# Kernel optimization log

Hardware: AMD Instinct MI355X
Metric: run time of the kernel (lower is better)

## Reference

```python
import jax, jax.numpy as jnp
import numpy as np

N = 1_048_576   # nodes
E = 8_388_608   # edges
G = 32_768      # graphs
D = 9           # node embedding dim (hardcoded emb_dim=9 in source)
H = 2 * D       # GIN MLP hidden
L = 3           # num_layers
ATOM_V, BOND_V = 119, 6
BN_EPS = 1e-5


def setup_inputs() -> dict:
    key = jax.random.key(0)
    ks = jax.random.split(key, 12)
    f = lambda i, shape: jax.random.normal(ks[i], shape, jnp.float32) * 0.1
    return {
        'atom_emb': f(0, (9, ATOM_V, D)),
        'bond_emb': f(1, (L, 3, BOND_V, D)),
        'eps_gin': jnp.zeros((L,), jnp.float32),
        'W1': f(2, (L, D, H)), 'b1': jnp.zeros((L, H)),
        'bn1_g': jnp.ones((L, H)), 'bn1_b': jnp.zeros((L, H)),
        'W2': f(3, (L, H, D)), 'b2': jnp.zeros((L, D)),
        'bno_g': jnp.ones((L, D)), 'bno_b': jnp.zeros((L, D)),
        'vnW1': f(4, (L - 1, D, H)), 'vnb1': jnp.zeros((L - 1, H)),
        'vnbn1_g': jnp.ones((L - 1, H)), 'vnbn1_b': jnp.zeros((L - 1, H)),
        'vnW2': f(5, (L - 1, H, D)), 'vnb2': jnp.zeros((L - 1, D)),
        'vnbn2_g': jnp.ones((L - 1, D)), 'vnbn2_b': jnp.zeros((L - 1, D)),
        'x': jax.random.randint(ks[6], (N, 9), 0, 2),
        'edge_index': jax.random.randint(ks[7], (2, E), 0, N),
        'edge_attr': jax.random.randint(ks[8], (E, 3), 0, 2),
        'batch': jnp.sort(jax.random.randint(ks[9], (N,), 0, G)),
        'num_graphs': G,
    }


def _bn(h, g, b):
    # BatchNorm1d in training mode: batch mean / biased variance
    m = h.mean(axis=0)
    v = h.var(axis=0)
    return (h - m) * jax.lax.rsqrt(v + BN_EPS) * g + b


def reference(atom_emb, bond_emb, eps_gin, W1, b1, bn1_g, bn1_b, W2, b2,
              bno_g, bno_b, vnW1, vnb1, vnbn1_g, vnbn1_b, vnW2, vnb2,
              vnbn2_g, vnbn2_b, x, edge_index, edge_attr, batch, num_graphs):
    n_nodes = x.shape[0]
    src, dst = edge_index[0], edge_index[1]
    # AtomEncoder: sum of per-field embeddings -> [N, D]
    h = atom_emb[jnp.arange(atom_emb.shape[0])[None, :], x].sum(axis=1)
    vn = jnp.zeros((num_graphs, h.shape[1]), h.dtype)  # virtualnode emb init 0
    num_layers = W1.shape[0]
    for l in range(num_layers):
        h_in = h + vn[batch]                              # broadcast VN to nodes
        # BondEncoder for this layer -> [E, D]
        e = bond_emb[l][jnp.arange(3)[None, :], edge_attr].sum(axis=1)
        # GIN message: relu(x_j + e), sum-aggregate at target
        msg = jax.nn.relu(h_in[src] + e)
        aggr = jax.ops.segment_sum(msg, dst, num_segments=n_nodes)
        z = (1.0 + eps_gin[l]) * h_in + aggr
        z = jax.nn.relu(_bn(z @ W1[l] + b1[l], bn1_g[l], bn1_b[l])) @ W2[l] + b2[l]
        z = _bn(z, bno_g[l], bno_b[l])
        if l < num_layers - 1:
            z = jax.nn.relu(z)
        h_new = z + h_in                                   # residual=True
        if l < num_layers - 1:
            vn_tmp = jax.ops.segment_sum(h_in, batch, num_segments=num_graphs) + vn
            t = jax.nn.relu(_bn(vn_tmp @ vnW1[l] + vnb1[l], vnbn1_g[l], vnbn1_b[l]))
            t = jax.nn.relu(_bn(t @ vnW2[l] + vnb2[l], vnbn2_g[l], vnbn2_b[l]))
            vn = vn + t                                    # VN residual
        h = h_new
    pooled = jax.ops.segment_sum(h, batch, num_segments=num_graphs)  # global_add_pool
    return jnp.sum(pooled, axis=0, keepdims=True)          # [1, D]
```

## Files before the change

### kernel.cpp

```cpp
#include <hip/hip_runtime.h>
#include <hip/hip_fp8.h>

#define NN 1048576
#define NE 8388608
#define NG 32768
#define DD 9
#define SB 12
#define HH 18
#define BN_EPS 1e-5f

#define NPB 512
#define NB  2048
#define NGRP 64
#define P3MAX 5120

#define NSUM1 0
#define NSQ1  18
#define NSUM2 36
#define NSQ2  45
#define OUTS  54
#define VBASE 4096
#define VSUM1 (VBASE+0)
#define VSQ1  (VBASE+18)
#define VSUM2 (VBASE+36)
#define VSQ2  (VBASE+45)
#define STATS_FLOATS 4224

typedef float fv4 __attribute__((ext_vector_type(4)));

__device__ __forceinline__ float waveReduce(float v) {
#pragma unroll
  for (int off = 32; off > 0; off >>= 1) v += __shfl_down(v, off, 64);
  return v;
}
__device__ __forceinline__ unsigned f8enc(float f) {
  __hip_fp8_e4m3 v(f);
  return (unsigned)v.__x;
}
__device__ __forceinline__ float f8dec(unsigned b) {
  __hip_fp8_e4m3 v;
  v.__x = (__hip_fp8_storage_t)b;
  return (float)v;
}


__global__ void k_count(const int* __restrict__ ei, int* __restrict__ bucket_count) {
  __shared__ int hist[NB];
  for (int i = threadIdx.x; i < NB; i += 256) hist[i] = 0;
  __syncthreads();
  const int CH = NE / 2048;
  int base = blockIdx.x * CH;
  for (int i = threadIdx.x; i < CH; i += 256)
    atomicAdd(&hist[ei[NE + base + i] >> 9], 1);
  __syncthreads();
  for (int i = threadIdx.x; i < NB; i += 256)
    if (hist[i]) atomicAdd(&bucket_count[i], hist[i]);
}

__global__ void k_scan(const int* __restrict__ bucket_count, int* __restrict__ bucket_base,
                       int* __restrict__ bucket_cursor, int* __restrict__ group_cursor) {
  __shared__ int tsum[256];
  int tid = threadIdx.x;
  int c[8];
  int run = 0;
#pragma unroll
  for (int k = 0; k < 8; ++k) { c[k] = bucket_count[tid * 8 + k]; run += c[k]; }
  tsum[tid] = run;
  __syncthreads();
  for (int off = 1; off < 256; off <<= 1) {
    int v = (tid >= off) ? tsum[tid - off] : 0;
    __syncthreads();
    tsum[tid] += v;
    __syncthreads();
  }
  int excl = tsum[tid] - run;
  if ((tid & 3) == 0) group_cursor[(tid >> 2) * 16] = excl;
#pragma unroll
  for (int k = 0; k < 8; ++k) {
    bucket_base[tid * 8 + k] = excl;
    bucket_cursor[tid * 8 + k] = excl;
    excl += c[k];
  }
  if (tid == 255) bucket_base[NB] = tsum[255];
}

#define P1K 32
__global__ void __launch_bounds__(256)
k_p1(const int* __restrict__ ei, const int* __restrict__ ea,
     int* __restrict__ group_cursor, uint2* __restrict__ coarse) {
  __shared__ uint2 stage[NGRP * P1K];
  __shared__ int scnt[NGRP], gbase[NGRP];
  int tid = threadIdx.x;
  for (int i = tid; i < NGRP; i += 256) scnt[i] = 0;
  __syncthreads();
  const int CH = NE / 2048;
  int base = blockIdx.x * CH;
  for (int batch = 0; batch < CH / 1024; ++batch) {
#pragma unroll
    for (int k = 0; k < 4; ++k) {
      int e = base + batch * 1024 + k * 256 + tid;
      int s = ei[e];
      int d = ei[NE + e];
      unsigned at = (unsigned)((ea[(size_t)e * 3 + 0] & 1) |
                               ((ea[(size_t)e * 3 + 1] & 1) << 1) |
                               ((ea[(size_t)e * 3 + 2] & 1) << 2));
      int g = d >> 14;
      uint2 rec = make_uint2((unsigned)s | (at << 20), (unsigned)d);
      int pos = atomicAdd(&scnt[g], 1);
      if (pos < P1K) stage[g * P1K + pos] = rec;
      else coarse[atomicAdd(&group_cursor[g * 16], 1)] = rec;
    }
    __syncthreads();
    {
      int g = tid >> 2, j = tid & 3;
      int cnt = min(scnt[g], P1K);
      if (j == 0) gbase[g] = cnt ? atomicAdd(&group_cursor[g * 16], cnt) : 0;
      __syncthreads();
      for (int i = j; i < cnt; i += 4) coarse[gbase[g] + i] = stage[g * P1K + i];
    }
    __syncthreads();
    if (tid < NGRP) scnt[tid] = 0;
    __syncthreads();
  }
}

#define P2K 48
#define P2SUB 32
__global__ void __launch_bounds__(256)
k_p2(const uint2* __restrict__ coarse, const int* __restrict__ bucket_base,
     int* __restrict__ bucket_cursor, unsigned* __restrict__ binned) {
  __shared__ unsigned stage[32 * P2K];
  __shared__ int scnt[32], gbase[32];
  int tid = threadIdx.x;
  int g = blockIdx.x >> 5;
  int sub = blockIdx.x & 31;
  int s0 = bucket_base[g << 5];
  int s1 = bucket_base[(g + 1) << 5];
  int len = s1 - s0;
  int chunk = (len + P2SUB - 1) >> 5;
  int my0 = s0 + sub * chunk;
  int my1 = min(my0 + chunk, s1);
  if (tid < 32) scnt[tid] = 0;
  __syncthreads();
  for (int b0 = my0; b0 < my1; b0 += 1024) {
#pragma unroll
    for (int k = 0; k < 4; ++k) {
      int i = b0 + k * 256 + tid;
      if (i < my1) {
        uint2 rec = coarse[i];
        unsigned s = rec.x & 0xFFFFFu;
        unsigned at = rec.x >> 20;
        unsigned d = rec.y;
        int bt = (int)((d >> 9) & 31u);
        unsigned o = s | ((d & 511u) << 20) | (at << 29);
        int pos = atomicAdd(&scnt[bt], 1);
        if (pos < P2K) stage[bt * P2K + pos] = o;
        else binned[atomicAdd(&bucket_cursor[(g << 5) | bt], 1)] = o;
      }
    }
    __syncthreads();
    {
      int bt = tid >> 3, j = tid & 7;
      int cnt = min(scnt[bt], P2K);
      if (j == 0) gbase[bt] = cnt ? atomicAdd(&bucket_cursor[(g << 5) | bt], cnt) : 0;
      __syncthreads();
      for (int i = j; i < cnt; i += 8) binned[gbase[bt] + i] = stage[bt * P2K + i];
    }
    __syncthreads();
    if (tid < 32) scnt[tid] = 0;
    __syncthreads();
  }
}

__global__ void __launch_bounds__(256)
k_p3(unsigned* __restrict__ binned, const int* __restrict__ bucket_base,
     int* __restrict__ row_ptr) {
  __shared__ int cnt[512];
  __shared__ int tsum[256];
  __shared__ unsigned stage[P3MAX];
  int tid = threadIdx.x;
  int b = blockIdx.x;
  int s0 = bucket_base[b], s1 = bucket_base[b + 1];
  int len = s1 - s0;
  for (int i = tid; i < 512; i += 256) cnt[i] = 0;
  __syncthreads();
  for (int i = tid; i < len; i += 256) {
    unsigned rec = binned[s0 + i];
    atomicAdd(&cnt[(rec >> 20) & 511u], 1);
  }
  __syncthreads();
  int c0 = cnt[2 * tid], c1 = cnt[2 * tid + 1];
  int run = c0 + c1;
  tsum[tid] = run;
  __syncthreads();
  for (int off = 1; off < 256; off <<= 1) {
    int v = (tid >= off) ? tsum[tid - off] : 0;
    __syncthreads();
    tsum[tid] += v;
    __syncthreads();
  }
  int excl = tsum[tid] - run;
  row_ptr[b * NPB + 2 * tid] = s0 + excl;
  row_ptr[b * NPB + 2 * tid + 1] = s0 + excl + c0;
  if (b == NB - 1 && tid == 255) row_ptr[NN] = s0 + excl + c0 + c1;
  __syncthreads();
  cnt[2 * tid] = excl;
  cnt[2 * tid + 1] = excl + c0;
  __syncthreads();
  for (int i = tid; i < len; i += 256) {
    unsigned rec = binned[s0 + i];
    int pos = atomicAdd(&cnt[(rec >> 20) & 511u], 1);
    stage[pos] = (rec & 0xFFFFFu) | ((rec >> 29) << 20);
  }
  __syncthreads();
  for (int i = tid; i < len; i += 256) binned[s0 + i] = stage[i];
}


__device__ __forceinline__ void writeMirror(uint2* __restrict__ hmA,
                                            unsigned char* __restrict__ hmB,
                                            size_t n, const float* hv) {
  uint2 q;
  q.x = f8enc(hv[0]) | (f8enc(hv[1]) << 8) | (f8enc(hv[2]) << 16) | (f8enc(hv[3]) << 24);
  q.y = f8enc(hv[4]) | (f8enc(hv[5]) << 8) | (f8enc(hv[6]) << 16) | (f8enc(hv[7]) << 24);
  hmA[n] = q;
  hmB[n] = (unsigned char)f8enc(hv[8]);
}

__global__ void k_atom(const float* __restrict__ atom_emb, const int* __restrict__ x,
                       const int* __restrict__ batch, float* __restrict__ h,
                       uint2* __restrict__ hmA, unsigned char* __restrict__ hmB,
                       float* __restrict__ vnsum) {
  int n = blockIdx.x * 256 + threadIdx.x;
  int xi[9];
#pragma unroll
  for (int f = 0; f < 9; ++f) xi[f] = x[(size_t)n * 9 + f];
  float acc[DD] = {0.f,0.f,0.f,0.f,0.f,0.f,0.f,0.f,0.f};
#pragma unroll
  for (int f = 0; f < 9; ++f) {
    const float* row = atom_emb + ((size_t)f * 119 + xi[f]) * DD;
#pragma unroll
    for (int d = 0; d < DD; ++d) acc[d] += row[d];
  }
  float* o = h + (size_t)n * SB;
  ((float4*)o)[0] = make_float4(acc[0], acc[1], acc[2], acc[3]);
  ((float4*)o)[1] = make_float4(acc[4], acc[5], acc[6], acc[7]);
  o[8] = acc[8];
  writeMirror(hmA, hmB, (size_t)n, acc);
  int g = batch[n];
  int lane = threadIdx.x & 63;
  float s[DD];
#pragma unroll
  for (int d = 0; d < DD; ++d) s[d] = acc[d];
#pragma unroll
  for (int st = 1; st < 64; st <<= 1) {
    int gu = __shfl_up(g, st, 64);
    bool ok = (lane >= st) && (gu == g);
#pragma unroll
    for (int d = 0; d < DD; ++d) {
      float vu = __shfl_up(s[d], st, 64);
      if (ok) s[d] += vu;
    }
  }
  int gn = __shfl_down(g, 1, 64);
  if ((lane == 63) || (gn != g)) {
#pragma unroll
    for (int d = 0; d < DD; ++d) atomicAdd(&vnsum[(size_t)g * DD + d], s[d]);
  }
}

__device__ __forceinline__ void edgeDecodeAcc(unsigned r, uint2 q, unsigned db,
                                              const float* __restrict__ comb,
                                              float* __restrict__ acc) {
  const float* cb = comb + (r >> 20) * DD;
  float hv[DD] = {f8dec(q.x & 255u), f8dec((q.x >> 8) & 255u),
                  f8dec((q.x >> 16) & 255u), f8dec(q.x >> 24),
                  f8dec(q.y & 255u), f8dec((q.y >> 8) & 255u),
                  f8dec((q.y >> 16) & 255u), f8dec(q.y >> 24),
                  f8dec(db)};
#pragma unroll
  for (int d = 0; d < DD; ++d) {
    float m = hv[d] + cb[d];
    m = m > 0.f ? m : 0.f;
    acc[d] += m;
  }
}

__device__ __forceinline__ void accumNode(const unsigned* __restrict__ binned,
                                          int e0, int e1,
                                          const uint2* __restrict__ hmA,
                                          const unsigned char* __restrict__ hmB,
                                          const float* __restrict__ comb,
                                          float* __restrict__ acc) {
  int i = e0;
  for (; i + 4 <= e1; i += 4) {
    unsigned r0 = binned[i], r1 = binned[i + 1], r2 = binned[i + 2], r3 = binned[i + 3];
    uint2 q0 = hmA[r0 & 0xFFFFFu];
    uint2 q1 = hmA[r1 & 0xFFFFFu];
    uint2 q2 = hmA[r2 & 0xFFFFFu];
    uint2 q3 = hmA[r3 & 0xFFFFFu];
    unsigned char d0 = hmB[r0 & 0xFFFFFu];
    unsigned char d1 = hmB[r1 & 0xFFFFFu];
    unsigned char d2 = hmB[r2 & 0xFFFFFu];
    unsigned char d3 = hmB[r3 & 0xFFFFFu];
    edgeDecodeAcc(r0, q0, d0, comb, acc);
    edgeDecodeAcc(r1, q1, d1, comb, acc);
    edgeDecodeAcc(r2, q2, d2, comb, acc);
    edgeDecodeAcc(r3, q3, d3, comb, acc);
  }
  for (; i < e1; ++i) {
    unsigned r = binned[i];
    uint2 q = hmA[r & 0xFFFFFu];
    unsigned char db = hmB[r & 0xFFFFFu];
    edgeDecodeAcc(r, q, db, comb, acc);
  }
}

__global__ void __launch_bounds__(256, 8)
k_edgeA(const float* __restrict__ hbuf, const uint2* __restrict__ hmA,
        const unsigned char* __restrict__ hmB, const unsigned* __restrict__ binned,
        const int* __restrict__ row_ptr, const float* __restrict__ bond,
        const float* __restrict__ W1l, const float* __restrict__ b1l,
        const float* __restrict__ epsp, float* __restrict__ X,
        float* __restrict__ stats) {
  __shared__ float comb[8 * DD];
  __shared__ float sW1[DD * HH], sb1[HH], ssum[HH], ssq[HH];
  int tid = threadIdx.x;
  for (int i = tid; i < DD * HH; i += 256) sW1[i] = W1l[i];
  if (tid < 8 * DD) {
    int c = tid / DD, d = tid % DD;
    comb[tid] = bond[(0 * 6 + (c & 1)) * DD + d] +
                bond[(1 * 6 + ((c >> 1) & 1)) * DD + d] +
                bond[(2 * 6 + ((c >> 2) & 1)) * DD + d];
  }
  if (tid < HH) { sb1[tid] = b1l[tid]; ssum[tid] = 0.f; ssq[tid] = 0.f; }
  __syncthreads();

  int b = blockIdx.x;
  int nA = b * NPB + tid;
  int nB = nA + 256;
  int ea0 = row_ptr[nA], ea1 = row_ptr[nA + 1];
  int eb0 = row_ptr[nB], eb1 = row_ptr[nB + 1];
  float acc0[DD] = {0.f,0.f,0.f,0.f,0.f,0.f,0.f,0.f,0.f};
  float acc1[DD] = {0.f,0.f,0.f,0.f,0.f,0.f,0.f,0.f,0.f};
  accumNode(binned, ea0, ea1, hmA, hmB, comb, acc0);
  accumNode(binned, eb0, eb1, hmA, hmB, comb, acc1);

  float eps1 = 1.0f + epsp[0];
  float z0[DD], z1[DD];
  {
    const float* hr = hbuf + (size_t)nA * SB;
    float4 HA = ((const float4*)hr)[0], HB = ((const float4*)hr)[1];
    float h8 = hr[8];
    float hi[DD] = {HA.x, HA.y, HA.z, HA.w, HB.x, HB.y, HB.z, HB.w, h8};
#pragma unroll
    for (int d = 0; d < DD; ++d) z0[d] = eps1 * hi[d] + acc0[d];
    float* xo = X + (size_t)nA * SB;
    fv4 v0 = {z0[0], z0[1], z0[2], z0[3]};
    fv4 v1 = {z0[4], z0[5], z0[6], z0[7]};
    __builtin_nontemporal_store(v0, (fv4*)xo);
    __builtin_nontemporal_store(v1, (fv4*)(xo + 4));
    __builtin_nontemporal_store(z0[8], xo + 8);
  }
  {
    const float* hr = hbuf + (size_t)nB * SB;
    float4 HA = ((const float4*)hr)[0], HB = ((const float4*)hr)[1];
    float h8 = hr[8];
    float hi[DD] = {HA.x, HA.y, HA.z, HA.w, HB.x, HB.y, HB.z, HB.w, h8};
#pragma unroll
    for (int d = 0; d < DD; ++d) z1[d] = eps1 * hi[d] + acc1[d];
    float* xo = X + (size_t)nB * SB;
    fv4 v0 = {z1[0], z1[1], z1[2], z1[3]};
    fv4 v1 = {z1[4], z1[5], z1[6], z1[7]};
    __builtin_nontemporal_store(v0, (fv4*)xo);
    __builtin_nontemporal_store(v1, (fv4*)(xo + 4));
    __builtin_nontemporal_store(z1[8], xo + 8);
  }
  int lane0 = ((tid & 63) == 0);
#pragma unroll
  for (int j = 0; j < HH; ++j) {
    float a0 = sb1[j], a1 = sb1[j];
#pragma unroll
    for (int d = 0; d < DD; ++d) {
      a0 += z0[d] * sW1[d * HH + j];
      a1 += z1[d] * sW1[d * HH + j];
    }
    float rs = waveReduce(a0 + a1);
    float rq = waveReduce(a0 * a0 + a1 * a1);
    if (lane0) { atomicAdd(&ssum[j], rs); atomicAdd(&ssq[j], rq); }
  }
  __syncthreads();
  int copy = (b & 63) * 64;
  if (tid < HH) {
    atomicAdd(&stats[copy + NSUM1 + tid], ssum[tid]);
    atomicAdd(&stats[copy + NSQ1 + tid], ssq[tid]);
  }
}

__global__ void __launch_bounds__(256)
k_partB(float* __restrict__ X, const float* __restrict__ W1l, const float* __restrict__ b1l,
        const float* __restrict__ g1, const float* __restrict__ be1,
        const float* __restrict__ W2l, const float* __restrict__ b2l,
        float* __restrict__ stats) {
  __shared__ float sW1[DD * HH], sW2[HH * DD], sb1[HH], sb2[DD];
  __shared__ float sc1[HH], sh1[HH], ssum[DD], ssq[DD];
  int tid = threadIdx.x;
  for (int i = tid; i < DD * HH; i += 256) sW1[i] = W1l[i];
  for (int i = tid; i < HH * DD; i += 256) sW2[i] = W2l[i];
  if (tid < HH) {
    float s = 0.f, q = 0.f;
#pragma unroll
    for (int c = 0; c < 64; ++c) {
      s += stats[c * 64 + NSUM1 + tid];
      q += stats[c * 64 + NSQ1 + tid];
    }
    float mean = s * (1.0f / NN);
    float var = q * (1.0f / NN) - mean * mean;
    float sc = g1[tid] * rsqrtf(var + BN_EPS);
    sc1[tid] = sc;
    sh1[tid] = be1[tid] - mean * sc;
    sb1[tid] = b1l[tid];
  }
  if (tid < DD) { sb2[tid] = b2l[tid]; ssum[tid] = 0.f; ssq[tid] = 0.f; }
  __syncthreads();
  size_t n = (size_t)blockIdx.x * 256 + tid;
  float* xr = X + n * SB;
  fv4 XA = __builtin_nontemporal_load((const fv4*)xr);
  fv4 XB = __builtin_nontemporal_load((const fv4*)(xr + 4));
  float x8 = __builtin_nontemporal_load(xr + 8);
  float z[DD] = {XA.x, XA.y, XA.z, XA.w, XB.x, XB.y, XB.z, XB.w, x8};
  float t[HH];
#pragma unroll
  for (int j = 0; j < HH; ++j) {
    float a = sb1[j];
#pragma unroll
    for (int d = 0; d < DD; ++d) a += z[d] * sW1[d * HH + j];
    a = a * sc1[j] + sh1[j];
    t[j] = a > 0.f ? a : 0.f;
  }
  float z2[DD];
  int lane0 = ((tid & 63) == 0);
#pragma unroll
  for (int d = 0; d < DD; ++d) {
    float a = sb2[d];
#pragma unroll
    for (int j = 0; j < HH; ++j) a += t[j] * sW2[j * DD + d];
    z2[d] = a;
    float rs = waveReduce(a);
    float rq = waveReduce(a * a);
    if (lane0) { atomicAdd(&ssum[d], rs); atomicAdd(&ssq[d], rq); }
  }
  fv4 v0 = {z2[0], z2[1], z2[2], z2[3]};
  fv4 v1 = {z2[4], z2[5], z2[6], z2[7]};
  __builtin_nontemporal_store(v0, (fv4*)xr);
  __builtin_nontemporal_store(v1, (fv4*)(xr + 4));
  __builtin_nontemporal_store(z2[8], xr + 8);
  __syncthreads();
  int copy = ((int)blockIdx.x & 63) * 64;
  if (tid < DD) {
    atomicAdd(&stats[copy + NSUM2 + tid], ssum[tid]);
    atomicAdd(&stats[copy + NSQ2 + tid], ssq[tid]);
  }
}

__global__ void __launch_bounds__(256)
k_partC(const float* __restrict__ X, float* __restrict__ hbuf,
        uint2* __restrict__ hmA, unsigned char* __restrict__ hmB,
        float* __restrict__ stats, const float* __restrict__ g2,
        const float* __restrict__ be2, const int* __restrict__ batch,
        const float* __restrict__ vn_next, float* __restrict__ vnsum_out,
        int do_relu) {
  __shared__ float sc[DD], sh[DD], ssum[DD];
  int tid = threadIdx.x;
  if (tid < DD) {
    float s = 0.f, q = 0.f;
#pragma unroll
    for (int c = 0; c < 64; ++c) {
      s += stats[c * 64 + NSUM2 + tid];
      q += stats[c * 64 + NSQ2 + tid];
    }
    float mean = s * (1.0f / NN);
    float var = q * (1.0f / NN) - mean * mean;
    float sg = g2[tid] * rsqrtf(var + BN_EPS);
    sc[tid] = sg;
    sh[tid] = be2[tid] - mean * sg;
    ssum[tid] = 0.f;
  }
  __syncthreads();
  size_t n = (size_t)blockIdx.x * 256 + tid;
  const float* xr = X + n * SB;
  fv4 XA = __builtin_nontemporal_load((const fv4*)xr);
  fv4 XB = __builtin_nontemporal_load((const fv4*)(xr + 4));
  float x8 = __builtin_nontemporal_load(xr + 8);
  float zv[DD] = {XA.x, XA.y, XA.z, XA.w, XB.x, XB.y, XB.z, XB.w, x8};
  float* hr = hbuf + n * SB;
  float4 HA = ((float4*)hr)[0], HB = ((float4*)hr)[1];
  float h8 = hr[8];
  float hi[DD] = {HA.x, HA.y, HA.z, HA.w, HB.x, HB.y, HB.z, HB.w, h8};
  float hv[DD];
#pragma unroll
  for (int d = 0; d < DD; ++d) {
    float z = zv[d] * sc[d] + sh[d];
    if (do_relu) z = z > 0.f ? z : 0.f;
    hv[d] = z + hi[d];
  }
  if (vn_next != nullptr) {
    int g = batch[n];
#pragma unroll
    for (int d = 0; d < DD; ++d) hv[d] += vn_next[(size_t)g * DD + d];
    ((float4*)hr)[0] = make_float4(hv[0], hv[1], hv[2], hv[3]);
    ((float4*)hr)[1] = make_float4(hv[4], hv[5], hv[6], hv[7]);
    hr[8] = hv[8];
    writeMirror(hmA, hmB, n, hv);
    if (vnsum_out != nullptr) {
      int lane = tid & 63;
      float s[DD];
#pragma unroll
      for (int d = 0; d < DD; ++d) s[d] = hv[d];
#pragma unroll
      for (int st = 1; st < 64; st <<= 1) {
        int gu = __shfl_up(g, st, 64);
        bool ok = (lane >= st) && (gu == g);
#pragma unroll
        for (int d = 0; d < DD; ++d) {
          float vu = __shfl_up(s[d], st, 64);
          if (ok) s[d] += vu;
        }
      }
      int gn = __shfl_down(g, 1, 64);
      if ((lane == 63) || (gn != g)) {
#pragma unroll
        for (int d = 0; d < DD; ++d) atomicAdd(&vnsum_out[(size_t)g * DD + d], s[d]);
      }
    }
  } else {
    int lane0 = ((tid & 63) == 0);
#pragma unroll
    for (int d = 0; d < DD; ++d) {
      float r = waveReduce(hv[d]);
      if (lane0) atomicAdd(&ssum[d], r);
    }
    __syncthreads();
    int copy = ((int)blockIdx.x & 63) * 64;
    if (tid < DD) atomicAdd(&stats[copy + OUTS + tid], ssum[tid]);
  }
}

__global__ void k_out(const float* __restrict__ stats, float* __restrict__ out) {
  int tid = threadIdx.x;
  if (tid < DD) {
    float s = 0.f;
#pragma unroll
    for (int c = 0; c < 64; ++c) s += stats[c * 64 + OUTS + tid];
    out[tid] = s;
  }
}


__global__ void k_vnA(const float* __restrict__ vnsum, const float* __restrict__ vn,
                      float* __restrict__ vt1, const float* __restrict__ W1l,
                      const float* __restrict__ b1l, float* __restrict__ stats) {
  __shared__ float sW[DD * HH], sb[HH], ssum[HH], ssq[HH];
  int tid = threadIdx.x;
  for (int i = tid; i < DD * HH; i += 256) sW[i] = W1l[i];
  if (tid < HH) { sb[tid] = b1l[tid]; ssum[tid] = 0.f; ssq[tid] = 0.f; }
  __syncthreads();
  size_t g = (size_t)blockIdx.x * 256 + tid;
  float r[DD];
#pragma unroll
  for (int d = 0; d < DD; ++d) r[d] = vnsum[g * DD + d] + vn[g * DD + d];
  int lane0 = ((tid & 63) == 0);
#pragma unroll
  for (int j = 0; j < HH; ++j) {
    float a = sb[j];
#pragma unroll
    for (int d = 0; d < DD; ++d) a += r[d] * sW[d * HH + j];
    vt1[g * HH + j] = a;
    float rs = waveReduce(a);
    float rq = waveReduce(a * a);
    if (lane0) { atomicAdd(&ssum[j], rs); atomicAdd(&ssq[j], rq); }
  }
  __syncthreads();
  if (tid < HH) {
    atomicAdd(&stats[VSUM1 + tid], ssum[tid]);
    atomicAdd(&stats[VSQ1 + tid], ssq[tid]);
  }
}

__global__ void k_vnB(const float* __restrict__ vt1, float* __restrict__ vt2,
                      const float* __restrict__ W2l, const float* __restrict__ b2l,
                      const float* __restrict__ g1, const float* __restrict__ be1,
                      float* __restrict__ stats) {
  __shared__ float sW2[HH * DD], sb2[DD], sc1[HH], sh1[HH], ssum[DD], ssq[DD];
  int tid = threadIdx.x;
  for (int i = tid; i < HH * DD; i += 256) sW2[i] = W2l[i];
  if (tid < HH) {
    float mean = stats[VSUM1 + tid] * (1.0f / NG);
    float var = stats[VSQ1 + tid] * (1.0f / NG) - mean * mean;
    float sc = g1[tid] * rsqrtf(var + BN_EPS);
    sc1[tid] = sc;
    sh1[tid] = be1[tid] - mean * sc;
  }
  if (tid < DD) { sb2[tid] = b2l[tid]; ssum[tid] = 0.f; ssq[tid] = 0.f; }
  __syncthreads();
  size_t g = (size_t)blockIdx.x * 256 + tid;
  float t[HH];
#pragma unroll
  for (int j = 0; j < HH; ++j) {
    float a = vt1[g * HH + j] * sc1[j] + sh1[j];
    t[j] = a > 0.f ? a : 0.f;
  }
  int lane0 = ((tid & 63) == 0);
#pragma unroll
  for (int d = 0; d < DD; ++d) {
    float a = sb2[d];
#pragma unroll
    for (int j = 0; j < HH; ++j) a += t[j] * sW2[j * DD + d];
    vt2[g * DD + d] = a;
    float rs = waveReduce(a);
    float rq = waveReduce(a * a);
    if (lane0) { atomicAdd(&ssum[d], rs); atomicAdd(&ssq[d], rq); }
  }
  __syncthreads();
  if (tid < DD) {
    atomicAdd(&stats[VSUM2 + tid], ssum[tid]);
    atomicAdd(&stats[VSQ2 + tid], ssq[tid]);
  }
}

__global__ void k_vnC(const float* __restrict__ vt2, float* __restrict__ vn,
                      const float* __restrict__ g2, const float* __restrict__ be2,
                      const float* __restrict__ stats) {
  __shared__ float sc[DD], sh[DD];
  int tid = threadIdx.x;
  if (tid < DD) {
    float mean = stats[VSUM2 + tid] * (1.0f / NG);
    float var = stats[VSQ2 + tid] * (1.0f / NG) - mean * mean;
    float s = g2[tid] * rsqrtf(var + BN_EPS);
    sc[tid] = s;
    sh[tid] = be2[tid] - mean * s;
  }
  __syncthreads();
  size_t g = (size_t)blockIdx.x * 256 + tid;
#pragma unroll
  for (int d = 0; d < DD; ++d) {
    float v = vt2[g * DD + d] * sc[d] + sh[d];
    v = v > 0.f ? v : 0.f;
    vn[g * DD + d] += v;
  }
}

extern "C" void kernel_launch(void* const* d_in, const int* in_sizes, int n_in,
                              void* d_out, int out_size, void* d_ws, size_t ws_size,
                              hipStream_t stream) {
  const float* atom_emb = (const float*)d_in[0];
  const float* bond_emb = (const float*)d_in[1];
  const float* eps_gin  = (const float*)d_in[2];
  const float* W1   = (const float*)d_in[3];
  const float* b1   = (const float*)d_in[4];
  const float* bn1_g = (const float*)d_in[5];
  const float* bn1_b = (const float*)d_in[6];
  const float* W2   = (const float*)d_in[7];
  const float* b2   = (const float*)d_in[8];
  const float* bno_g = (const float*)d_in[9];
  const float* bno_b = (const float*)d_in[10];
  const float* vnW1 = (const float*)d_in[11];
  const float* vnb1 = (const float*)d_in[12];
  const float* vnbn1_g = (const float*)d_in[13];
  const float* vnbn1_b = (const float*)d_in[14];
  const float* vnW2 = (const float*)d_in[15];
  const float* vnb2 = (const float*)d_in[16];
  const float* vnbn2_g = (const float*)d_in[17];
  const float* vnbn2_b = (const float*)d_in[18];
  const int* x          = (const int*)d_in[19];
  const int* edge_index = (const int*)d_in[20];
  const int* edge_attr  = (const int*)d_in[21];
  const int* batch      = (const int*)d_in[22];
  float* out = (float*)d_out;

  float* hbuf  = (float*)d_ws;
  float* X     = hbuf + (size_t)NN * SB;
  uint2* hmA   = (uint2*)(X + (size_t)NN * SB);
  unsigned char* hmB = (unsigned char*)(hmA + (size_t)NN);
  unsigned* binned = (unsigned*)(hmB + (size_t)NN);
  uint2* coarse = (uint2*)d_ws;
  float* vn    = (float*)(binned + (size_t)NE);
  float* vnsum = vn + (size_t)NG * DD;
  float* vt2   = vnsum;
  float* vt1   = vnsum + (size_t)NG * DD;
  float* stats = vt1 + (size_t)NG * HH;
  int* bucket_count  = (int*)(stats + STATS_FLOATS);
  int* bucket_base   = bucket_count + NB;
  int* bucket_cursor = bucket_base + NB + 1;
  int* group_cursor  = bucket_cursor + NB;
  int* row_ptr       = group_cursor + NGRP * 16;

  (void)hipMemsetAsync(bucket_count, 0, NB * sizeof(int), stream);
  k_count<<<2048, 256, 0, stream>>>(edge_index, bucket_count);
  k_scan<<<1, 256, 0, stream>>>(bucket_count, bucket_base, bucket_cursor, group_cursor);
  k_p1<<<2048, 256, 0, stream>>>(edge_index, edge_attr, group_cursor, coarse);
  k_p2<<<NGRP * P2SUB, 256, 0, stream>>>(coarse, bucket_base, bucket_cursor, binned);
  k_p3<<<NB, 256, 0, stream>>>(binned, bucket_base, row_ptr);

  (void)hipMemsetAsync(vn, 0, (size_t)2 * NG * DD * sizeof(float), stream);
  k_atom<<<NN / 256, 256, 0, stream>>>(atom_emb, x, batch, hbuf, hmA, hmB, vnsum);

  for (int l = 0; l < 3; ++l) {
    int has_vn = (l < 2);
    (void)hipMemsetAsync(stats, 0, STATS_FLOATS * sizeof(float), stream);
    if (has_vn) {
      k_vnA<<<NG / 256, 256, 0, stream>>>(vnsum, vn, vt1, vnW1 + (size_t)l * DD * HH,
                                          vnb1 + (size_t)l * HH, stats);
      k_vnB<<<NG / 256, 256, 0, stream>>>(vt1, vt2, vnW2 + (size_t)l * HH * DD,
                                          vnb2 + (size_t)l * DD,
                                          vnbn1_g + (size_t)l * HH, vnbn1_b + (size_t)l * HH,
                                          stats);
      k_vnC<<<NG / 256, 256, 0, stream>>>(vt2, vn, vnbn2_g + (size_t)l * DD,
                                          vnbn2_b + (size_t)l * DD, stats);
    }
    k_edgeA<<<NB, 256, 0, stream>>>(hbuf, hmA, hmB, binned, row_ptr,
                                    bond_emb + (size_t)l * 3 * 6 * DD,
                                    W1 + (size_t)l * DD * HH, b1 + (size_t)l * HH,
                                    eps_gin + l, X, stats);
    k_partB<<<NN / 256, 256, 0, stream>>>(X, W1 + (size_t)l * DD * HH,
                                          b1 + (size_t)l * HH,
                                          bn1_g + (size_t)l * HH, bn1_b + (size_t)l * HH,
                                          W2 + (size_t)l * HH * DD, b2 + (size_t)l * DD,
                                          stats);
    if (l == 0)
      (void)hipMemsetAsync(vnsum, 0, (size_t)NG * DD * sizeof(float), stream);
    k_partC<<<NN / 256, 256, 0, stream>>>(X, hbuf, hmA, hmB, stats,
                                          bno_g + (size_t)l * DD, bno_b + (size_t)l * DD,
                                          batch,
                                          has_vn ? vn : nullptr,
                                          (l == 0) ? vnsum : nullptr,
                                          has_vn ? 1 : 0);
  }
  k_out<<<1, 64, 0, stream>>>(stats, out);
}
```

Measured before the change: 1.415 ms.

## Replace atomic-cursor coarse scatter with per-block prefix offsets for deterministic partition

The count pass now also records per-block, per-group edge counts, and a new scan kernel turns them into exclusive offsets. Edge partitioning into 64 coarse groups can then write directly to precomputed positions using only shared-memory counters. This removes the global atomic cursors and the shared staging and flush loop in the first partition pass. Global bucket counters are padded to separate cache lines to reduce atomic contention. The cost is one extra small scan launch, a per-block count table in the workspace, and a change to 512 blocks of 1024 threads.

```diff
diff --git a/kernel.cpp b/kernel.cpp
--- a/kernel.cpp
+++ b/kernel.cpp
@@ -12,6 +12,7 @@
 #define NPB 512
 #define NB  2048
 #define NGRP 64
+#define P1B 512
 #define P3MAX 5120
 
 #define NSUM1 0
@@ -44,27 +45,36 @@
 }
 
 
-__global__ void k_count(const int* __restrict__ ei, int* __restrict__ bucket_count) {
+__global__ void __launch_bounds__(1024)
+k_counthist(const int* __restrict__ ei, int* __restrict__ cnt_pad,
+            int* __restrict__ blkcnt) {
   __shared__ int hist[NB];
-  for (int i = threadIdx.x; i < NB; i += 256) hist[i] = 0;
-  __syncthreads();
-  const int CH = NE / 2048;
+  int tid = threadIdx.x;
+  for (int i = tid; i < NB; i += 1024) hist[i] = 0;
+  __syncthreads();
+  const int CH = NE / P1B;
   int base = blockIdx.x * CH;
-  for (int i = threadIdx.x; i < CH; i += 256)
+  for (int i = tid; i < CH; i += 1024)
     atomicAdd(&hist[ei[NE + base + i] >> 9], 1);
   __syncthreads();
-  for (int i = threadIdx.x; i < NB; i += 256)
-    if (hist[i]) atomicAdd(&bucket_count[i], hist[i]);
-}
-
-__global__ void k_scan(const int* __restrict__ bucket_count, int* __restrict__ bucket_base,
-                       int* __restrict__ bucket_cursor, int* __restrict__ group_cursor) {
+  for (int i = tid; i < NB; i += 1024)
+    if (hist[i]) atomicAdd(&cnt_pad[i * 16], hist[i]);
+  if (tid < NGRP) {
+    int s = 0;
+#pragma unroll
+    for (int k = 0; k < 32; ++k) s += hist[tid * 32 + k];
+    blkcnt[tid * P1B + blockIdx.x] = s;
+  }
+}
+
+__global__ void k_scan(const int* __restrict__ cnt_pad, int* __restrict__ bucket_base,
+                       int* __restrict__ bucket_cursor) {
   __shared__ int tsum[256];
   int tid = threadIdx.x;
   int c[8];
   int run = 0;
 #pragma unroll
-  for (int k = 0; k < 8; ++k) { c[k] = bucket_count[tid * 8 + k]; run += c[k]; }
+  for (int k = 0; k < 8; ++k) { c[k] = cnt_pad[(tid * 8 + k) * 16]; run += c[k]; }
   tsum[tid] = run;
   __syncthreads();
   for (int off = 1; off < 256; off <<= 1) {
@@ -74,7 +84,6 @@
     __syncthreads();
   }
   int excl = tsum[tid] - run;
-  if ((tid & 3) == 0) group_cursor[(tid >> 2) * 16] = excl;
 #pragma unroll
   for (int k = 0; k < 8; ++k) {
     bucket_base[tid * 8 + k] = excl;
@@ -84,43 +93,45 @@
   if (tid == 255) bucket_base[NB] = tsum[255];
 }
 
-#define P1K 32
-__global__ void __launch_bounds__(256)
+__global__ void k_scanG(int* __restrict__ blkcnt, const int* __restrict__ bucket_base) {
+  __shared__ int tsum[256];
+  int tid = threadIdx.x;
+  int g = blockIdx.x;
+  int c0 = blkcnt[g * P1B + 2 * tid], c1 = blkcnt[g * P1B + 2 * tid + 1];
+  int run = c0 + c1;
+  tsum[tid] = run;
+  __syncthreads();
+  for (int off = 1; off < 256; off <<= 1) {
+    int v = (tid >= off) ? tsum[tid - off] : 0;
+    __syncthreads();
+    tsum[tid] += v;
+    __syncthreads();
+  }
+  int excl = tsum[tid] - run + bucket_base[g << 5];
+  blkcnt[g * P1B + 2 * tid] = excl;
+  blkcnt[g * P1B + 2 * tid + 1] = excl + c0;
+}
+
+__global__ void __launch_bounds__(1024)
 k_p1(const int* __restrict__ ei, const int* __restrict__ ea,
-     int* __restrict__ group_cursor, uint2* __restrict__ coarse) {
-  __shared__ uint2 stage[NGRP * P1K];
-  __shared__ int scnt[NGRP], gbase[NGRP];
-  int tid = threadIdx.x;
-  for (int i = tid; i < NGRP; i += 256) scnt[i] = 0;
-  __syncthreads();
-  const int CH = NE / 2048;
+     const int* __restrict__ blkcnt, uint2* __restrict__ coarse) {
+  __shared__ int lcnt[NGRP];
+  __shared__ int lbase[NGRP];
+  int tid = threadIdx.x;
+  if (tid < NGRP) { lcnt[tid] = 0; lbase[tid] = blkcnt[tid * P1B + blockIdx.x]; }
+  __syncthreads();
+  const int CH = NE / P1B;
   int base = blockIdx.x * CH;
-  for (int batch = 0; batch < CH / 1024; ++batch) {
-#pragma unroll
-    for (int k = 0; k < 4; ++k) {
-      int e = base + batch * 1024 + k * 256 + tid;
-      int s = ei[e];
-      int d = ei[NE + e];
-      unsigned at = (unsigned)((ea[(size_t)e * 3 + 0] & 1) |
-                               ((ea[(size_t)e * 3 + 1] & 1) << 1) |
-                               ((ea[(size_t)e * 3 + 2] & 1) << 2));
-      int g = d >> 14;
-      uint2 rec = make_uint2((unsigned)s | (at << 20), (unsigned)d);
-      int pos = atomicAdd(&scnt[g], 1);
-      if (pos < P1K) stage[g * P1K + pos] = rec;
-      else coarse[atomicAdd(&group_cursor[g * 16], 1)] = rec;
-    }
-    __syncthreads();
-    {
-      int g = tid >> 2, j = tid & 3;
-      int cnt = min(scnt[g], P1K);
-      if (j == 0) gbase[g] = cnt ? atomicAdd(&group_cursor[g * 16], cnt) : 0;
-      __syncthreads();
-      for (int i = j; i < cnt; i += 4) coarse[gbase[g] + i] = stage[g * P1K + i];
-    }
-    __syncthreads();
-    if (tid < NGRP) scnt[tid] = 0;
-    __syncthreads();
+  for (int k = 0; k < CH / 1024; ++k) {
+    int e = base + k * 1024 + tid;
+    int s = ei[e];
+    int d = ei[NE + e];
+    unsigned at = (unsigned)((ea[(size_t)e * 3 + 0] & 1) |
+                             ((ea[(size_t)e * 3 + 1] & 1) << 1) |
+                             ((ea[(size_t)e * 3 + 2] & 1) << 2));
+    int g = d >> 14;
+    int pos = atomicAdd(&lcnt[g], 1);
+    coarse[lbase[g] + pos] = make_uint2((unsigned)s | (at << 20), (unsigned)d);
   }
 }
 
@@ -683,22 +694,23 @@
   uint2* hmA   = (uint2*)(X + (size_t)NN * SB);
   unsigned char* hmB = (unsigned char*)(hmA + (size_t)NN);
   unsigned* binned = (unsigned*)(hmB + (size_t)NN);
-  uint2* coarse = (uint2*)d_ws;
   float* vn    = (float*)(binned + (size_t)NE);
   float* vnsum = vn + (size_t)NG * DD;
   float* vt2   = vnsum;
   float* vt1   = vnsum + (size_t)NG * DD;
   float* stats = vt1 + (size_t)NG * HH;
-  int* bucket_count  = (int*)(stats + STATS_FLOATS);
-  int* bucket_base   = bucket_count + NB;
+  int* bucket_base   = (int*)(stats + STATS_FLOATS);
   int* bucket_cursor = bucket_base + NB + 1;
-  int* group_cursor  = bucket_cursor + NB;
-  int* row_ptr       = group_cursor + NGRP * 16;
-
-  (void)hipMemsetAsync(bucket_count, 0, NB * sizeof(int), stream);
-  k_count<<<2048, 256, 0, stream>>>(edge_index, bucket_count);
-  k_scan<<<1, 256, 0, stream>>>(bucket_count, bucket_base, bucket_cursor, group_cursor);
-  k_p1<<<2048, 256, 0, stream>>>(edge_index, edge_attr, group_cursor, coarse);
+  int* row_ptr       = bucket_cursor + NB;
+  uint2* coarse = (uint2*)d_ws;
+  int* cnt_pad  = (int*)((char*)d_ws + (size_t)NE * sizeof(uint2));
+  int* blkcnt   = cnt_pad + (size_t)NB * 16;
+
+  (void)hipMemsetAsync(cnt_pad, 0, (size_t)NB * 16 * sizeof(int), stream);
+  k_counthist<<<P1B, 1024, 0, stream>>>(edge_index, cnt_pad, blkcnt);
+  k_scan<<<1, 256, 0, stream>>>(cnt_pad, bucket_base, bucket_cursor);
+  k_scanG<<<NGRP, 256, 0, stream>>>(blkcnt, bucket_base);
+  k_p1<<<P1B, 1024, 0, stream>>>(edge_index, edge_attr, blkcnt, coarse);
   k_p2<<<NGRP * P2SUB, 256, 0, stream>>>(coarse, bucket_base, bucket_cursor, binned);
   k_p3<<<NB, 256, 0, stream>>>(binned, bucket_base, row_ptr);
 
```

Result: faster. 1.343 ms (-5.1%).
